# Kernel tuning notes

Hardware: AMD Instinct MI355X
Metric: run time of the kernel (lower is better)

## Reference

```python
import math
import jax, jax.numpy as jnp
import numpy as np

B, T, D, HS = 8, 2048, 1024, 64  # batch, seq (== block_size), d_embed, head_size
BLOCK_SIZE = 2048


def setup_inputs() -> dict:
    key = jax.random.key(0)
    kx, kq, kk, kv = jax.random.split(key, 4)
    x = jax.random.normal(kx, (B, T, D), dtype=jnp.float32)
    Wq = jax.random.normal(kq, (D, HS), dtype=jnp.float32) * (1.0 / math.sqrt(D))
    Wk = jax.random.normal(kk, (D, HS), dtype=jnp.float32) * (1.0 / math.sqrt(D))
    Wv = jax.random.normal(kv, (D, HS), dtype=jnp.float32) * (1.0 / math.sqrt(D))
    return {"x": x, "Wq": Wq, "Wk": Wk, "Wv": Wv}


def reference(x, Wq, Wk, Wv):
    # q, k, v: [B, T, HS]
    q = jnp.einsum("btd,dh->bth", x, Wq)
    k = jnp.einsum("btd,dh->bth", x, Wk)
    v = jnp.einsum("btd,dh->bth", x, Wv)
    # NOTE: original scales by 1/sqrt(block_size), not 1/sqrt(head_size)
    scale = 1.0 / math.sqrt(BLOCK_SIZE)
    scores = jnp.einsum("bqh,bkh->bqk", q, k) * scale  # [B, T, T]
    Tq = x.shape[1]
    causal = jnp.tril(jnp.ones((Tq, Tq), dtype=bool))
    scores = jnp.where(causal[None, :, :], scores, -jnp.inf)
    attn = jax.nn.softmax(scores, axis=-1)
    return jnp.einsum("bqk,bkh->bqh", attn, v)  # [B, T, HS]
```

## Files before the change

### kernel.cpp

```cpp
#include <hip/hip_runtime.h>

typedef unsigned short u16;
typedef unsigned int u32;
typedef float f32x4 __attribute__((ext_vector_type(4)));
typedef short s16x8 __attribute__((ext_vector_type(8)));

#define MFMA_BF16(a, b, c) __builtin_amdgcn_mfma_f32_16x16x32_bf16((a), (b), (c), 0, 0, 0)


__device__ __forceinline__ u16 f2bf(float f) {
  union { float f; u32 u; } v; v.f = f;
  u32 u = v.u;
  return (u16)((u + 0x7FFFu + ((u >> 16) & 1u)) >> 16);
}
__device__ __forceinline__ u16 f2bf_t(float f) {
  union { float f; u32 u; } v; v.f = f;
  return (u16)(v.u >> 16);
}
__device__ __forceinline__ s16x8 pack_bf8(float4 a, float4 b) {
  union { u32 d[4]; s16x8 v; } u;
  u.d[0] = (u32)f2bf(a.x) | ((u32)f2bf(a.y) << 16);
  u.d[1] = (u32)f2bf(a.z) | ((u32)f2bf(a.w) << 16);
  u.d[2] = (u32)f2bf(b.x) | ((u32)f2bf(b.y) << 16);
  u.d[3] = (u32)f2bf(b.z) | ((u32)f2bf(b.w) << 16);
  return u.v;
}
__device__ __forceinline__ void gload_lds16(const void* g, void* l) {
  __builtin_amdgcn_global_load_lds((const __attribute__((address_space(1))) u32*)g,
                                   (__attribute__((address_space(3))) u32*)l, 16, 0, 0);
}

__global__ __launch_bounds__(256) void wt_convert(const float* __restrict__ Wq,
                                                  const float* __restrict__ Wk,
                                                  const float* __restrict__ Wv,
                                                  u16* __restrict__ Wt3) {
  __shared__ u16 Ls[64][70];
  const int bid = blockIdx.x;
  const int m = bid >> 4, kstep = bid & 15, d0 = kstep * 64;
  const float* W = (m == 0) ? Wq : (m == 1) ? Wk : Wv;
  const int t = threadIdx.x;
  {
    const int dr = t >> 2, hc = (t & 3) * 16;
    const float4* src = (const float4*)(W + (size_t)(d0 + dr) * 64 + hc);
    float4 f0 = src[0], f1 = src[1], f2 = src[2], f3 = src[3];
    float fl[16] = {f0.x, f0.y, f0.z, f0.w, f1.x, f1.y, f1.z, f1.w,
                    f2.x, f2.y, f2.z, f2.w, f3.x, f3.y, f3.z, f3.w};
#pragma unroll
    for (int j = 0; j < 8; ++j) {
      u32 pk = (u32)f2bf(fl[2 * j]) | ((u32)f2bf(fl[2 * j + 1]) << 16);
      *(u32*)&Ls[dr][hc + 2 * j] = pk;
    }
  }
  __syncthreads();
  {
    const int h = t >> 2, dcs = (t & 3) * 16;
    const int grow = m * 64 + h;
    u32 po[8];
#pragma unroll
    for (int j = 0; j < 8; ++j)
      po[j] = (u32)Ls[dcs + 2 * j][h] | ((u32)Ls[dcs + 2 * j + 1][h] << 16);
    u16* dst = Wt3 + (size_t)kstep * 12288 + grow * 64 + dcs;
    *(uint4*)&dst[0] = make_uint4(po[0], po[1], po[2], po[3]);
    *(uint4*)&dst[8] = make_uint4(po[4], po[5], po[6], po[7]);
  }
}

__global__ __launch_bounds__(1024) void qkv_gemm(const float* __restrict__ x,
                                                 const u16* __restrict__ Wt3,
                                                 u16* __restrict__ qo,
                                                 u16* __restrict__ ko,
                                                 u16* __restrict__ vTo) {
  __shared__ float Xf[2][4096];
  __shared__ u16 Wl[2][12288];
  const int tid = threadIdx.x, lane = tid & 63, w = tid >> 6;
  const int lc = lane & 15, hi = lane >> 4;
  const int m0 = blockIdx.x * 64;
  const int msub = w & 3, ntg = w >> 2;

  f32x4 acc[3];
#pragma unroll
  for (int i = 0; i < 3; ++i) acc[i] = (f32x4){0.f, 0.f, 0.f, 0.f};

  const int rX = w * 4 + (lane >> 4);
  const int gX = (lane & 15) ^ (rX & 15);
  const float* xsrc = x + (size_t)(m0 + rX) * 1024 + gX * 4;
  const int rW = w * 8 + (lane >> 3);
  const int gW = (lane & 7) ^ (rW & 7);
  const u16* wsrc = Wt3 + rW * 64 + gW * 8;

  auto stage = [&](int t, int bf) {
    gload_lds16(xsrc + t * 64, &Xf[bf][w * 256]);
    gload_lds16(wsrc + (size_t)t * 12288, &Wl[bf][w * 512]);
    if (w < 8) gload_lds16(wsrc + (size_t)t * 12288 + 8192, &Wl[bf][(16 + w) * 512]);
  };

  stage(0, 0);
  __syncthreads();
  int buf = 0;

  const int rA = msub * 16 + lc;
  for (int t = 0; t < 16; ++t) {
    if (t < 15) stage(t + 1, buf ^ 1);
#pragma unroll
    for (int ksub = 0; ksub < 2; ++ksub) {
      const int g0 = ksub * 8 + hi * 2;
      float4 alo = *(const float4*)&Xf[buf][rA * 64 + ((g0 ^ (rA & 15)) << 2)];
      float4 ahi = *(const float4*)&Xf[buf][rA * 64 + (((g0 + 1) ^ (rA & 15)) << 2)];
      s16x8 a = pack_bf8(alo, ahi);
#pragma unroll
      for (int j = 0; j < 3; ++j) {
        const int rB = (ntg * 3 + j) * 16 + lc;
        const int gB = (ksub * 4 + hi) ^ (rB & 7);
        s16x8 b = *(const s16x8*)&Wl[buf][rB * 64 + gB * 8];
        acc[j] = MFMA_BF16(a, b, acc[j]);
      }
    }
    if (t < 15) {
      __syncthreads();
      buf ^= 1;
    }
  }

#pragma unroll
  for (int j = 0; j < 3; ++j) {
    const int nt = ntg * 3 + j;
#pragma unroll
    for (int r = 0; r < 4; ++r) {
      const int gr = m0 + msub * 16 + hi * 4 + r;
      const u16 val = f2bf(acc[j][r]);
      const int n = nt * 16 + lc;
      if (nt < 4) {
        qo[gr * 64 + n] = val;
      } else if (nt < 8) {
        ko[gr * 64 + (n - 64)] = val;
      } else {
        int b = gr >> 11, t2 = gr & 2047;
        vTo[((b << 6) + (n - 128)) * 2048 + t2] = val;
      }
    }
  }
}

__global__ __launch_bounds__(256, 2) void attn_fwd(const u16* __restrict__ qb,
                                                   const u16* __restrict__ kb,
                                                   const u16* __restrict__ vT,
                                                   float* __restrict__ out) {
  __shared__ float PoS[4][32][66];
  __shared__ float Pl[4][32];
  const int tid = threadIdx.x, lane = tid & 63, w = tid >> 6;
  const int lc = lane & 15, hi = lane >> 4;
  const int bid = blockIdx.x;
  const int b = bid & 7, v = 63 - (bid >> 3);
  const int q0 = v * 32;
  const int brow = b * 2048;
  u16* Pw = (u16*)&PoS[w][0][0];

  s16x8 aq[2][2];
#pragma unroll
  for (int sub = 0; sub < 2; ++sub) {
    const u16* qrow = qb + (size_t)(brow + q0 + sub * 16 + lc) * 64;
    aq[sub][0] = *(const s16x8*)(qrow + hi * 8);
    aq[sub][1] = *(const s16x8*)(qrow + 32 + hi * 8);
  }

  f32x4 o[2][4];
  float lrow[2][4];
#pragma unroll
  for (int sub = 0; sub < 2; ++sub)
#pragma unroll
    for (int i = 0; i < 4; ++i) {
      o[sub][i] = (f32x4){0.f, 0.f, 0.f, 0.f};
      lrow[sub][i] = 0.f;
    }

  const float SL = 0.031879357f;
  const int nk = v + 1;
  const int c = (nk + 3) >> 2;
  const int s = w;
  const int it0 = s * c;
  const int it1 = min(it0 + c, nk);

  const u16* kbase = kb + (size_t)brow * 64;

  for (int it = it0; it < it1; ++it) {
    const int kvb = it * 32;
    const u16* krow0 = kbase + (size_t)(kvb + lc) * 64;
    const u16* krow1 = kbase + (size_t)(kvb + 16 + lc) * 64;
    s16x8 k00 = *(const s16x8*)(krow0 + hi * 8);
    s16x8 k01 = *(const s16x8*)(krow0 + 32 + hi * 8);
    s16x8 k10 = *(const s16x8*)(krow1 + hi * 8);
    s16x8 k11 = *(const s16x8*)(krow1 + 32 + hi * 8);
    s16x8 bv[4];
#pragma unroll
    for (int nt = 0; nt < 4; ++nt)
      bv[nt] = *(const s16x8*)&vT[(size_t)(b * 64 + nt * 16 + lc) * 2048 + kvb + hi * 8];

    f32x4 sc[2][2];
#pragma unroll
    for (int sub = 0; sub < 2; ++sub) {
      sc[sub][0] = (f32x4){0.f, 0.f, 0.f, 0.f};
      sc[sub][1] = (f32x4){0.f, 0.f, 0.f, 0.f};
      sc[sub][0] = MFMA_BF16(aq[sub][0], k00, sc[sub][0]);
      sc[sub][0] = MFMA_BF16(aq[sub][1], k01, sc[sub][0]);
      sc[sub][1] = MFMA_BF16(aq[sub][0], k10, sc[sub][1]);
      sc[sub][1] = MFMA_BF16(aq[sub][1], k11, sc[sub][1]);
    }

    if (kvb + 31 <= q0) {
#pragma unroll
      for (int sub = 0; sub < 2; ++sub)
#pragma unroll
        for (int r = 0; r < 4; ++r) {
          float p0 = exp2f(sc[sub][0][r] * SL);
          float p1 = exp2f(sc[sub][1][r] * SL);
          lrow[sub][r] += p0 + p1;
          Pw[(sub * 16 + hi * 4 + r) * 40 + lc] = f2bf_t(p0);
          Pw[(sub * 16 + hi * 4 + r) * 40 + 16 + lc] = f2bf_t(p1);
        }
    } else {
#pragma unroll
      for (int sub = 0; sub < 2; ++sub)
#pragma unroll
        for (int r = 0; r < 4; ++r) {
          const int qt = q0 + sub * 16 + hi * 4 + r;
          const int kv0 = kvb + lc;
          float p0 = (kv0 <= qt) ? exp2f(sc[sub][0][r] * SL) : 0.f;
          float p1 = (kv0 + 16 <= qt) ? exp2f(sc[sub][1][r] * SL) : 0.f;
          lrow[sub][r] += p0 + p1;
          Pw[(sub * 16 + hi * 4 + r) * 40 + lc] = f2bf_t(p0);
          Pw[(sub * 16 + hi * 4 + r) * 40 + 16 + lc] = f2bf_t(p1);
        }
    }
    asm volatile("s_waitcnt lgkmcnt(0)" ::: "memory");
    s16x8 pa0 = *(const s16x8*)&Pw[lc * 40 + hi * 8];
    s16x8 pa1 = *(const s16x8*)&Pw[(16 + lc) * 40 + hi * 8];
#pragma unroll
    for (int nt = 0; nt < 4; ++nt) {
      o[0][nt] = MFMA_BF16(pa0, bv[nt], o[0][nt]);
      o[1][nt] = MFMA_BF16(pa1, bv[nt], o[1][nt]);
    }
  }

#pragma unroll
  for (int sub = 0; sub < 2; ++sub)
#pragma unroll
    for (int r = 0; r < 4; ++r) {
      float l = lrow[sub][r];
      l += __shfl_xor(l, 1);
      l += __shfl_xor(l, 2);
      l += __shfl_xor(l, 4);
      l += __shfl_xor(l, 8);
      lrow[sub][r] = l;
    }

  if (lc == 0) {
#pragma unroll
    for (int sub = 0; sub < 2; ++sub)
#pragma unroll
      for (int r = 0; r < 4; ++r) Pl[w][sub * 16 + hi * 4 + r] = lrow[sub][r];
  }
  float* Pow = &PoS[w][0][0];
#pragma unroll
  for (int sub = 0; sub < 2; ++sub)
#pragma unroll
    for (int nt = 0; nt < 4; ++nt)
#pragma unroll
      for (int r = 0; r < 4; ++r)
        Pow[(sub * 16 + hi * 4 + r) * 66 + nt * 16 + lc] = o[sub][nt][r];
  __syncthreads();

#pragma unroll
  for (int rr = 0; rr < 8; ++rr) {
    const int row = w * 8 + rr;
    float L = Pl[0][row] + Pl[1][row] + Pl[2][row] + Pl[3][row];
    float val = PoS[0][row][lane] + PoS[1][row][lane] + PoS[2][row][lane] + PoS[3][row][lane];
    out[(size_t)(brow + q0 + row) * 64 + lane] = val / L;
  }
}

extern "C" void kernel_launch(void* const* d_in, const int* in_sizes, int n_in,
                              void* d_out, int out_size, void* d_ws, size_t ws_size,
                              hipStream_t stream) {
  (void)in_sizes; (void)n_in; (void)out_size; (void)ws_size;
  const float* x = (const float*)d_in[0];
  const float* Wq = (const float*)d_in[1];
  const float* Wk = (const float*)d_in[2];
  const float* Wv = (const float*)d_in[3];
  float* out = (float*)d_out;

  u16* wsu = (u16*)d_ws;
  u16* Wt = wsu;
  u16* qb = Wt + 192 * 1024;
  u16* kb = qb + 8 * 2048 * 64;
  u16* vT = kb + 8 * 2048 * 64;

  wt_convert<<<48, 256, 0, stream>>>(Wq, Wk, Wv, Wt);
  qkv_gemm<<<256, 1024, 0, stream>>>(x, Wt, qb, kb, vT);
  attn_fwd<<<512, 256, 0, stream>>>(qb, kb, vT, out);
}
```

Baseline: 58.80 us.

## Deepen QKV GEMM pipeline to four-stage k=32 ring with vmcnt waits

```diff
diff --git a/kernel.cpp b/kernel.cpp
--- a/kernel.cpp
+++ b/kernel.cpp
@@ -36,7 +36,7 @@
                                                   u16* __restrict__ Wt3) {
   __shared__ u16 Ls[64][70];
   const int bid = blockIdx.x;
-  const int m = bid >> 4, kstep = bid & 15, d0 = kstep * 64;
+  const int m = bid >> 4, d0 = (bid & 15) * 64;
   const float* W = (m == 0) ? Wq : (m == 1) ? Wk : Wv;
   const int t = threadIdx.x;
   {
@@ -55,11 +55,12 @@
   {
     const int h = t >> 2, dcs = (t & 3) * 16;
     const int grow = m * 64 + h;
+    const int dd = d0 + dcs;
     u32 po[8];
 #pragma unroll
     for (int j = 0; j < 8; ++j)
       po[j] = (u32)Ls[dcs + 2 * j][h] | ((u32)Ls[dcs + 2 * j + 1][h] << 16);
-    u16* dst = Wt3 + (size_t)kstep * 12288 + grow * 64 + dcs;
+    u16* dst = Wt3 + ((size_t)(dd >> 5) * 192 + grow) * 32 + (dd & 31);
     *(uint4*)&dst[0] = make_uint4(po[0], po[1], po[2], po[3]);
     *(uint4*)&dst[8] = make_uint4(po[4], po[5], po[6], po[7]);
   }
@@ -70,8 +71,8 @@
                                                  u16* __restrict__ qo,
                                                  u16* __restrict__ ko,
                                                  u16* __restrict__ vTo) {
-  __shared__ float Xf[2][4096];
-  __shared__ u16 Wl[2][12288];
+  __shared__ float Xf[4][2048];
+  __shared__ u16 Wl[4][6144];
   const int tid = threadIdx.x, lane = tid & 63, w = tid >> 6;
   const int lc = lane & 15, hi = lane >> 4;
   const int m0 = blockIdx.x * 64;
@@ -81,44 +82,58 @@
 #pragma unroll
   for (int i = 0; i < 3; ++i) acc[i] = (f32x4){0.f, 0.f, 0.f, 0.f};
 
-  const int rX = w * 4 + (lane >> 4);
-  const int gX = (lane & 15) ^ (rX & 15);
-  const float* xsrc = x + (size_t)(m0 + rX) * 1024 + gX * 4;
-  const int rW = w * 8 + (lane >> 3);
-  const int gW = (lane & 7) ^ (rW & 7);
-  const u16* wsrc = Wt3 + rW * 64 + gW * 8;
+  const int xrow = (w & 7) * 8 + (lane >> 3);
+  const int xg = (lane & 7) ^ ((lane >> 3) & 7);
+  const float* xsrc = x + (size_t)(m0 + xrow) * 1024 + xg * 4;
+  const int j1 = (w >= 8) ? (w - 8) : (8 + w);
+  const int wrow1 = j1 * 16 + (lane >> 2);
+  const int gW = (lane & 3) ^ ((lane >> 2) & 3) ^ ((lane >> 4) & 3);
+  const u16* wsrc = Wt3 + wrow1 * 32 + gW * 8;
+  const bool sx = (w < 8), sw = (w >= 8) || (w < 4);
 
   auto stage = [&](int t, int bf) {
-    gload_lds16(xsrc + t * 64, &Xf[bf][w * 256]);
-    gload_lds16(wsrc + (size_t)t * 12288, &Wl[bf][w * 512]);
-    if (w < 8) gload_lds16(wsrc + (size_t)t * 12288 + 8192, &Wl[bf][(16 + w) * 512]);
+    if (sx) gload_lds16(xsrc + (size_t)t * 32, &Xf[bf][(w & 7) * 256]);
+    if (sw) gload_lds16(wsrc + (size_t)t * 6144, &Wl[bf][j1 * 512]);
   };
 
+  const int rA = msub * 16 + lc;
+  const int aof0 = rA * 32 + ((((hi * 2)) ^ (rA & 7)) << 2);
+  const int aof1 = rA * 32 + ((((hi * 2) + 1) ^ (rA & 7)) << 2);
+  int bof[3];
+#pragma unroll
+  for (int j = 0; j < 3; ++j) {
+    const int rB = (ntg * 3 + j) * 16 + lc;
+    const int slot = hi ^ (rB & 3) ^ ((rB >> 2) & 3);
+    bof[j] = rB * 32 + slot * 8;
+  }
+
   stage(0, 0);
-  __syncthreads();
-  int buf = 0;
-
-  const int rA = msub * 16 + lc;
-  for (int t = 0; t < 16; ++t) {
-    if (t < 15) stage(t + 1, buf ^ 1);
-#pragma unroll
-    for (int ksub = 0; ksub < 2; ++ksub) {
-      const int g0 = ksub * 8 + hi * 2;
-      float4 alo = *(const float4*)&Xf[buf][rA * 64 + ((g0 ^ (rA & 15)) << 2)];
-      float4 ahi = *(const float4*)&Xf[buf][rA * 64 + (((g0 + 1) ^ (rA & 15)) << 2)];
-      s16x8 a = pack_bf8(alo, ahi);
-#pragma unroll
-      for (int j = 0; j < 3; ++j) {
-        const int rB = (ntg * 3 + j) * 16 + lc;
-        const int gB = (ksub * 4 + hi) ^ (rB & 7);
-        s16x8 b = *(const s16x8*)&Wl[buf][rB * 64 + gB * 8];
-        acc[j] = MFMA_BF16(a, b, acc[j]);
-      }
-    }
-    if (t < 15) {
-      __syncthreads();
-      buf ^= 1;
-    }
+  stage(1, 1);
+  stage(2, 2);
+
+  for (int t = 0; t < 32; ++t) {
+    if (t <= 29) {
+      if (w < 4) asm volatile("s_waitcnt vmcnt(4)" ::: "memory");
+      else       asm volatile("s_waitcnt vmcnt(2)" ::: "memory");
+    } else if (t == 30) {
+      if (w < 4) asm volatile("s_waitcnt vmcnt(2)" ::: "memory");
+      else       asm volatile("s_waitcnt vmcnt(1)" ::: "memory");
+    } else {
+      asm volatile("s_waitcnt vmcnt(0)" ::: "memory");
+    }
+    asm volatile("s_waitcnt lgkmcnt(0)" ::: "memory");
+    __builtin_amdgcn_s_barrier();
+    __builtin_amdgcn_sched_barrier(0);
+    const int bf = t & 3;
+    float4 alo = *(const float4*)&Xf[bf][aof0];
+    float4 ahi = *(const float4*)&Xf[bf][aof1];
+    s16x8 a = pack_bf8(alo, ahi);
+#pragma unroll
+    for (int j = 0; j < 3; ++j) {
+      s16x8 bfr = *(const s16x8*)&Wl[bf][bof[j]];
+      acc[j] = MFMA_BF16(a, bfr, acc[j]);
+    }
+    if (t < 29) stage(t + 3, (t + 3) & 3);
   }
 
 #pragma unroll
```

After: 57.32 us. 1.03x faster.

## Shrink QKV GEMM tiles to 32 rows and K-step 32 for more blocks

Applied to the files above, without the earlier changes.

```diff
diff --git a/kernel.cpp b/kernel.cpp
--- a/kernel.cpp
+++ b/kernel.cpp
@@ -1,4 +1,5 @@
 #include <hip/hip_runtime.h>
+#include <hip/hip_bf16.h>
 
 typedef unsigned short u16;
 typedef unsigned int u32;
@@ -18,12 +19,12 @@
   return (u16)(v.u >> 16);
 }
 __device__ __forceinline__ s16x8 pack_bf8(float4 a, float4 b) {
-  union { u32 d[4]; s16x8 v; } u;
-  u.d[0] = (u32)f2bf(a.x) | ((u32)f2bf(a.y) << 16);
-  u.d[1] = (u32)f2bf(a.z) | ((u32)f2bf(a.w) << 16);
-  u.d[2] = (u32)f2bf(b.x) | ((u32)f2bf(b.y) << 16);
-  u.d[3] = (u32)f2bf(b.z) | ((u32)f2bf(b.w) << 16);
-  return u.v;
+  union { __hip_bfloat162 h2[4]; s16x8 s; } u;
+  u.h2[0] = __float22bfloat162_rn(make_float2(a.x, a.y));
+  u.h2[1] = __float22bfloat162_rn(make_float2(a.z, a.w));
+  u.h2[2] = __float22bfloat162_rn(make_float2(b.x, b.y));
+  u.h2[3] = __float22bfloat162_rn(make_float2(b.z, b.w));
+  return u.s;
 }
 __device__ __forceinline__ void gload_lds16(const void* g, void* l) {
   __builtin_amdgcn_global_load_lds((const __attribute__((address_space(1))) u32*)g,
@@ -36,7 +37,7 @@
                                                   u16* __restrict__ Wt3) {
   __shared__ u16 Ls[64][70];
   const int bid = blockIdx.x;
-  const int m = bid >> 4, kstep = bid & 15, d0 = kstep * 64;
+  const int m = bid >> 4, d0 = (bid & 15) * 64;
   const float* W = (m == 0) ? Wq : (m == 1) ? Wk : Wv;
   const int t = threadIdx.x;
   {
@@ -55,67 +56,72 @@
   {
     const int h = t >> 2, dcs = (t & 3) * 16;
     const int grow = m * 64 + h;
+    const int dd = d0 + dcs;
     u32 po[8];
 #pragma unroll
     for (int j = 0; j < 8; ++j)
       po[j] = (u32)Ls[dcs + 2 * j][h] | ((u32)Ls[dcs + 2 * j + 1][h] << 16);
-    u16* dst = Wt3 + (size_t)kstep * 12288 + grow * 64 + dcs;
+    u16* dst = Wt3 + ((size_t)(dd >> 5) * 192 + grow) * 32 + (dd & 31);
     *(uint4*)&dst[0] = make_uint4(po[0], po[1], po[2], po[3]);
     *(uint4*)&dst[8] = make_uint4(po[4], po[5], po[6], po[7]);
   }
 }
 
-__global__ __launch_bounds__(1024) void qkv_gemm(const float* __restrict__ x,
-                                                 const u16* __restrict__ Wt3,
-                                                 u16* __restrict__ qo,
-                                                 u16* __restrict__ ko,
-                                                 u16* __restrict__ vTo) {
-  __shared__ float Xf[2][4096];
-  __shared__ u16 Wl[2][12288];
+__global__ __launch_bounds__(512) void qkv_gemm(const float* __restrict__ x,
+                                                const u16* __restrict__ Wt3,
+                                                u16* __restrict__ qo,
+                                                u16* __restrict__ ko,
+                                                u16* __restrict__ vTo) {
+  __shared__ float Xf[2][1024];
+  __shared__ u16 Wl[2][6144];
   const int tid = threadIdx.x, lane = tid & 63, w = tid >> 6;
   const int lc = lane & 15, hi = lane >> 4;
-  const int m0 = blockIdx.x * 64;
-  const int msub = w & 3, ntg = w >> 2;
+  const int m0 = blockIdx.x * 32;
+  const int msub = w & 1, ntg = w >> 1;
 
   f32x4 acc[3];
 #pragma unroll
   for (int i = 0; i < 3; ++i) acc[i] = (f32x4){0.f, 0.f, 0.f, 0.f};
 
-  const int rX = w * 4 + (lane >> 4);
-  const int gX = (lane & 15) ^ (rX & 15);
-  const float* xsrc = x + (size_t)(m0 + rX) * 1024 + gX * 4;
-  const int rW = w * 8 + (lane >> 3);
-  const int gW = (lane & 7) ^ (rW & 7);
-  const u16* wsrc = Wt3 + rW * 64 + gW * 8;
+  const int xrow = tid >> 3;
+  const int xgs = (tid & 7) ^ ((tid >> 3) & 7);
+  const float* xsrc = x + (size_t)(m0 + xrow) * 1024 + xgs * 4;
+  const int w0r = tid >> 2, w0g = (tid & 3) ^ ((tid >> 3) & 3);
+  const int c1 = tid + 512;
+  const int w1r = c1 >> 2, w1g = (c1 & 3) ^ ((c1 >> 3) & 3);
 
   auto stage = [&](int t, int bf) {
-    gload_lds16(xsrc + t * 64, &Xf[bf][w * 256]);
-    gload_lds16(wsrc + (size_t)t * 12288, &Wl[bf][w * 512]);
-    if (w < 8) gload_lds16(wsrc + (size_t)t * 12288 + 8192, &Wl[bf][(16 + w) * 512]);
+    if (tid < 256) gload_lds16(xsrc + (size_t)t * 32, &Xf[bf][tid * 4]);
+    gload_lds16(Wt3 + (size_t)t * 6144 + w0r * 32 + w0g * 8, &Wl[bf][tid * 8]);
+    if (tid < 256)
+      gload_lds16(Wt3 + (size_t)t * 6144 + w1r * 32 + w1g * 8, &Wl[bf][c1 * 8]);
   };
+
+  const int rA = msub * 16 + lc;
+  const int aof0 = rA * 32 + (((hi * 2) ^ (rA & 7)) << 2);
+  const int aof1 = rA * 32 + (((hi * 2 + 1) ^ (rA & 7)) << 2);
+  int bof[3];
+#pragma unroll
+  for (int j = 0; j < 3; ++j) {
+    const int rB = (ntg * 3 + j) * 16 + lc;
+    bof[j] = rB * 32 + ((hi ^ ((rB >> 1) & 3)) << 3);
+  }
 
   stage(0, 0);
   __syncthreads();
   int buf = 0;
 
-  const int rA = msub * 16 + lc;
-  for (int t = 0; t < 16; ++t) {
-    if (t < 15) stage(t + 1, buf ^ 1);
-#pragma unroll
-    for (int ksub = 0; ksub < 2; ++ksub) {
-      const int g0 = ksub * 8 + hi * 2;
-      float4 alo = *(const float4*)&Xf[buf][rA * 64 + ((g0 ^ (rA & 15)) << 2)];
-      float4 ahi = *(const float4*)&Xf[buf][rA * 64 + (((g0 + 1) ^ (rA & 15)) << 2)];
-      s16x8 a = pack_bf8(alo, ahi);
-#pragma unroll
-      for (int j = 0; j < 3; ++j) {
-        const int rB = (ntg * 3 + j) * 16 + lc;
-        const int gB = (ksub * 4 + hi) ^ (rB & 7);
-        s16x8 b = *(const s16x8*)&Wl[buf][rB * 64 + gB * 8];
-        acc[j] = MFMA_BF16(a, b, acc[j]);
-      }
-    }
-    if (t < 15) {
+  for (int t = 0; t < 32; ++t) {
+    if (t < 31) stage(t + 1, buf ^ 1);
+    float4 alo = *(const float4*)&Xf[buf][aof0];
+    float4 ahi = *(const float4*)&Xf[buf][aof1];
+    s16x8 a = pack_bf8(alo, ahi);
+#pragma unroll
+    for (int j = 0; j < 3; ++j) {
+      s16x8 bfr = *(const s16x8*)&Wl[buf][bof[j]];
+      acc[j] = MFMA_BF16(a, bfr, acc[j]);
+    }
+    if (t < 31) {
       __syncthreads();
       buf ^= 1;
     }
@@ -295,6 +301,6 @@
   u16* vT = kb + 8 * 2048 * 64;
 
   wt_convert<<<48, 256, 0, stream>>>(Wq, Wk, Wv, Wt);
-  qkv_gemm<<<256, 1024, 0, stream>>>(x, Wt, qb, kb, vT);
+  qkv_gemm<<<512, 512, 0, stream>>>(x, Wt, qb, kb, vT);
   attn_fwd<<<512, 256, 0, stream>>>(qb, kb, vT, out);
 }
```

Result: faster. 57.47 us (-2.3%).
